# Performance work log

Measured on AMD Instinct MI355X. Metric: run time of the kernel, lower is better.

The kernel has to match this reference:

```python
import jax, jax.numpy as jnp
import numpy as np

B, N, NC = 16, 128, 32          # batch, num_vectors, num_condition_vectors
H, A, DEG = 256, 64, 3          # hidden_dim, attention_dim, degree
SCALE = float(np.sqrt(H) ** DEG)  # weights_scale = sqrt(hidden_dim)^degree = 4096
# S3 non-identity permutations lifted to batch tensor axes (batch axis 0 fixed)
PERMS = [(0, 1, 3, 2), (0, 2, 1, 3), (0, 2, 3, 1), (0, 3, 1, 2), (0, 3, 2, 1)]


def setup_inputs() -> dict:
    key = jax.random.key(0)
    ks = jax.random.split(key, 6)
    inv = 1.0 / np.sqrt(H)
    return {
        "x": jax.random.normal(ks[0], (B, N, H), jnp.float32),
        "x_mask": jnp.ones((B, N, 1), jnp.float32),
        "condition": jax.random.normal(ks[1], (B, NC, H), jnp.float32),
        "condition_mask": jnp.ones((B, NC, 1), jnp.float32),
        "W1": (jax.random.normal(ks[2], (DEG, H, H), jnp.float32) * inv),
        "b1": jnp.zeros((DEG, H), jnp.float32),
        "Wc": (jax.random.normal(ks[3], (DEG, H, H), jnp.float32) * inv),
        "Wlin": (jax.random.normal(ks[4], (DEG, H, A), jnp.float32) * inv),
        "blin": jnp.zeros((DEG, A), jnp.float32),
    }


def reference(x, x_mask, condition, condition_mask, W1, b1, Wc, Wlin, blin):
    # masked mean-pool of condition vectors: [B, H]
    pooled = (condition * condition_mask).sum(1) / jnp.maximum(condition_mask.sum(1), 1.0)
    ys, dvs = [], []
    for d in range(DEG):  # small fixed loop over structurally distinct branches
        dv = pooled @ Wc[d]                                   # daughter vector [B, H]
        h = jax.nn.gelu(x @ W1[d] + b1[d] + dv[:, None, :])   # branch encoder [B, N, H]
        y = (h @ Wlin[d] + blin[d]) * x_mask                  # linear + mask  [B, N, A]
        ys.append(y)
        dvs.append(dv)
    # degree-3 multilinear contraction: 'xbi,ybi,zbi->bxyz' == 'bxi,byi,bzi->bxyz'
    base = jnp.einsum('bxi,byi,bzi->bxyz', ys[0], ys[1], ys[2]) / SCALE
    # symmetrize: add all non-identity permuted views (S3 minus identity)
    out = base
    for p in PERMS:
        out = out + jnp.transpose(base, p)
    return out, jnp.stack(dvs)  # ([B,N,N,N], [DEG,B,H])
```

## Files before the change

### kernel.cpp

```cpp
#include <hip/hip_runtime.h>
#include <hip/hip_bf16.h>
#include <math.h>
#include <string.h>

#define BB   16
#define NN   128
#define NCC  32
#define HH   256
#define AA   64
#define DEGN 3
#define BNR  (BB*NN)

typedef __bf16 bf16x8 __attribute__((ext_vector_type(8)));
typedef float  f32x16 __attribute__((ext_vector_type(16)));

__device__ __forceinline__ unsigned int pk2(float lo, float hi) {
    __hip_bfloat162 h2 = __float22bfloat162_rn(make_float2(lo, hi));
    unsigned int u;
    memcpy(&u, &h2, 4);
    return u;
}
__device__ __forceinline__ unsigned short bfbits(float f) {
    __hip_bfloat16 h = __float2bfloat16(f);
    unsigned short u;
    memcpy(&u, &h, 2);
    return u;
}

__global__ __launch_bounds__(256) void k_head(const float* __restrict__ cond,
                                              const float* __restrict__ cmask,
                                              const float* __restrict__ Wc,
                                              const float* __restrict__ W1,
                                              const float* __restrict__ Wlin,
                                              float* __restrict__ dv,
                                              float* __restrict__ dv_out,
                                              unsigned short* __restrict__ W1t,
                                              unsigned short* __restrict__ Wlt) {
    __shared__ float shm[32 * 33];
    const int bid = blockIdx.x, t = threadIdx.x;

    if (bid < 48) {
        const int d = bid >> 4, b = bid & 15;
        float s = 0.f, ms = 0.f;
        for (int c = 0; c < NCC; ++c) {
            float mk = cmask[b * NCC + c];
            s  += cond[(b * NCC + c) * HH + t] * mk;
            ms += mk;
        }
        shm[t] = s / fmaxf(ms, 1.0f);
        __syncthreads();
        const float* Wd = Wc + (size_t)d * HH * HH;
        float acc = 0.f;
        for (int k = 0; k < HH; ++k) acc += shm[k] * Wd[k * HH + t];
        int idx = (d * BB + b) * HH + t;
        dv[idx]     = acc;
        dv_out[idx] = acc;
    } else if (bid < 240) {
        const int q = bid - 48;
        const int d = q >> 6, r2 = q & 63, tk = r2 >> 3, tn = r2 & 7;
        float (*tile)[33] = (float (*)[33])shm;
        #pragma unroll
        for (int p = 0; p < 4; ++p) {
            int kr = p * 8 + (t >> 5), nr = t & 31;
            tile[kr][nr] = W1[((size_t)d * HH + tk * 32 + kr) * HH + tn * 32 + nr];
        }
        __syncthreads();
        #pragma unroll
        for (int p = 0; p < 4; ++p) {
            int nr = p * 8 + (t >> 5), kr = t & 31;
            W1t[((size_t)d * HH + tn * 32 + nr) * HH + tk * 32 + kr] =
                bfbits(tile[kr][nr]);
        }
    } else {
        const int q = bid - 240;
        const int d = q >> 4, r3 = q & 15, tk = r3 >> 1, ta = r3 & 1;
        float (*tile)[33] = (float (*)[33])shm;
        #pragma unroll
        for (int p = 0; p < 4; ++p) {
            int kr = p * 8 + (t >> 5), ar = t & 31;
            tile[kr][ar] = Wlin[((size_t)d * HH + tk * 32 + kr) * AA + ta * 32 + ar];
        }
        __syncthreads();
        #pragma unroll
        for (int p = 0; p < 4; ++p) {
            int ar = p * 8 + (t >> 5), kr = t & 31;
            Wlt[((size_t)d * AA + ta * 32 + ar) * HH + tk * 32 + kr] =
                bfbits(tile[kr][ar]);
        }
    }
}

__global__ __launch_bounds__(256) void k_mlp(const float* __restrict__ x,
                                             const float* __restrict__ xmask,
                                             const float* __restrict__ b1,
                                             const float* __restrict__ blin,
                                             const float* __restrict__ dv,
                                             const unsigned short* __restrict__ W1t,
                                             const unsigned short* __restrict__ Wlt,
                                             float* __restrict__ yv) {
    __shared__ __align__(16) char ldsA[32 * 512];
    __shared__ float ps[2][32][68];

    const int t = threadIdx.x;
    const int d = blockIdx.x >> 6, rt = blockIdx.x & 63;
    const int row0 = rt * 32;
    const int b = row0 >> 7;
    const int lane = t & 63, wid = t >> 6;
    const int rl5 = lane & 31, h2v = lane >> 5;

    #pragma unroll
    for (int it = 0; it < 8; ++it) {
        const int r = wid * 8 + it;
        const float4 v = *(const float4*)&x[(size_t)(row0 + r) * HH + lane * 4];
        uint2 u = make_uint2(pk2(v.x, v.y), pk2(v.z, v.w));
        *(uint2*)(ldsA + r * 512 + ((lane * 8) ^ ((r & 7) << 4))) = u;
    }
    __syncthreads();

    f32x16 acc1[2];
    #pragma unroll
    for (int nt = 0; nt < 2; ++nt)
        #pragma unroll
        for (int e = 0; e < 16; ++e) acc1[nt][e] = 0.f;

    #pragma unroll
    for (int ks = 0; ks < 16; ++ks) {
        bf16x8 af = *(const bf16x8*)(ldsA + rl5 * 512 +
                      ((ks * 32 + h2v * 16) ^ ((rl5 & 7) << 4)));
        #pragma unroll
        for (int nt = 0; nt < 2; ++nt) {
            const int n = wid * 64 + nt * 32 + rl5;
            bf16x8 bf = *(const bf16x8*)(W1t +
                          ((size_t)d * HH + n) * HH + ks * 16 + h2v * 8);
            acc1[nt] = __builtin_amdgcn_mfma_f32_32x32x16_bf16(af, bf, acc1[nt], 0, 0, 0);
        }
    }
    __syncthreads();

    #pragma unroll
    for (int nt = 0; nt < 2; ++nt) {
        const int col = wid * 64 + nt * 32 + rl5;
        const float add = b1[d * HH + col] + dv[(d * BB + b) * HH + col];
        #pragma unroll
        for (int e = 0; e < 16; ++e) {
            const int row = (e & 3) + 8 * (e >> 2) + 4 * h2v;
            float v = acc1[nt][e] + add;
            float u = 0.7978845608028654f * (v + 0.044715f * v * v * v);
            float g = 0.5f * v * (1.0f + tanhf(u));
            *(unsigned short*)(ldsA + row * 512 + ((col * 2) ^ ((row & 7) << 4))) =
                bfbits(g);
        }
    }
    __syncthreads();

    const int qc = wid >> 1, kh = wid & 1;
    f32x16 acc2;
    #pragma unroll
    for (int e = 0; e < 16; ++e) acc2[e] = 0.f;
    #pragma unroll
    for (int ks = 0; ks < 8; ++ks) {
        const int kk = kh * 8 + ks;
        bf16x8 af = *(const bf16x8*)(ldsA + rl5 * 512 +
                      ((kk * 32 + h2v * 16) ^ ((rl5 & 7) << 4)));
        bf16x8 bf = *(const bf16x8*)(Wlt +
                      ((size_t)d * AA + qc * 32 + rl5) * HH + kk * 16 + h2v * 8);
        acc2 = __builtin_amdgcn_mfma_f32_32x32x16_bf16(af, bf, acc2, 0, 0, 0);
    }
    #pragma unroll
    for (int e = 0; e < 16; ++e) {
        const int row = (e & 3) + 8 * (e >> 2) + 4 * h2v;
        ps[kh][row][qc * 32 + rl5] = acc2[e];
    }
    __syncthreads();

    #pragma unroll
    for (int j = 0; j < 8; ++j) {
        const int idx = t * 8 + j;
        const int row = idx >> 6, a = idx & 63;
        float v = ps[0][row][a] + ps[1][row][a] + blin[d * AA + a];
        v *= xmask[row0 + row];
        yv[((size_t)d * BNR + row0 + row) * AA + a] = v;
    }
}

__device__ __forceinline__ void lds_fence_barrier() {
    asm volatile("s_waitcnt lgkmcnt(0)" ::: "memory");
    __builtin_amdgcn_s_barrier();
    __builtin_amdgcn_sched_barrier(0);
}
__device__ __forceinline__ void lds_wave_wait() {
    asm volatile("s_waitcnt lgkmcnt(0)" ::: "memory");
    __builtin_amdgcn_sched_barrier(0);
}

#define LROW 128

__global__ __launch_bounds__(256, 2) void k_contract(const float* __restrict__ yv,
                                                     float* __restrict__ outp) {
    __shared__ __align__(16) char lds[4 * 128 * LROW];
    char* A1b = lds;
    char* A2b = lds + 1 * 128 * LROW;
    char* B1b = lds + 2 * 128 * LROW;
    char* B2b = lds + 3 * 128 * LROW;

    const int t  = threadIdx.x;
    const int b  = blockIdx.x >> 5;
    const int xg = blockIdx.x & 31;

    const float* y0p = yv + (size_t)(0 * BNR + b * NN) * AA;
    const float* y1p = yv + (size_t)(1 * BNR + b * NN) * AA;
    const float* y2p = yv + (size_t)(2 * BNR + b * NN) * AA;

    const int lane = t & 63;
    const int wid  = t >> 6;
    const int li   = lane & 31;
    const int rh   = lane >> 5;

    #pragma unroll
    for (int it = 0; it < 16; ++it) {
        const int r   = wid * 32 + it * 2 + rh;
        const int swz = (r & 7) << 4;
        const float2 v1 = *(const float2*)&y1p[r * AA + 2 * li];
        const float2 v2 = *(const float2*)&y2p[r * AA + 2 * li];
        *(unsigned int*)(B1b + r * LROW + ((4 * li) ^ swz)) = pk2(v2.x, v2.y);
        *(unsigned int*)(B2b + r * LROW + ((4 * li) ^ swz)) = pk2(v1.x, v1.y);
    }

    const int rl5 = lane & 31, h2v = lane >> 5;
    const int wy  = wid * 32;
    const float inv = 1.0f / 4096.0f;

    char* s1 = A1b + wid * 4096;
    char* s2 = A2b + wid * 4096;

    for (int xi = 0; xi < 4; ++xi) {
        const int xr = xg * 4 + xi;
        const float s0 = y0p[xr * AA + lane];
        const float s1v = y1p[xr * AA + lane];
        const float s2v = y2p[xr * AA + lane];
        const float s0a = __shfl(s0, 2 * li),  s0b = __shfl(s0, 2 * li + 1);
        const float s1a = __shfl(s1v, 2 * li), s1b = __shfl(s1v, 2 * li + 1);
        const float s2a = __shfl(s2v, 2 * li), s2b = __shfl(s2v, 2 * li + 1);

        #pragma unroll
        for (int it = 0; it < 16; ++it) {
            const int r   = wid * 32 + it * 2 + rh;
            const int swz = (r & 7) << 4;
            const float2 v0 = *(const float2*)&y0p[r * AA + 2 * li];
            const float2 v1 = *(const float2*)&y1p[r * AA + 2 * li];
            unsigned int a1 = pk2(s0a * v1.x + s1a * v0.x, s0b * v1.y + s1b * v0.y);
            unsigned int a2 = pk2(s2a * v0.x, s2b * v0.y);
            *(unsigned int*)(A1b + r * LROW + ((4 * li) ^ swz)) = a1;
            *(unsigned int*)(A2b + r * LROW + ((4 * li) ^ swz)) = a2;
        }
        lds_fence_barrier();

        f32x16 acc[4];
        #pragma unroll
        for (int ni = 0; ni < 4; ++ni)
            #pragma unroll
            for (int e = 0; e < 16; ++e) acc[ni][e] = 0.f;

        #pragma unroll
        for (int p = 0; p < 4; ++p) {
            const char* Ua = (p == 0) ? A1b : (p == 1) ? B1b : (p == 2) ? A2b : B2b;
            const char* Va = (p == 0) ? B1b : (p == 1) ? A1b : (p == 2) ? B2b : A2b;
            #pragma unroll
            for (int ks = 0; ks < 4; ++ks) {
                const int arow = wy + rl5;
                bf16x8 af = *(const bf16x8*)(Ua + arow * LROW +
                              ((ks * 32 + h2v * 16) ^ ((arow & 7) << 4)));
                #pragma unroll
                for (int ni = 0; ni < 4; ++ni) {
                    const int brow = ni * 32 + rl5;
                    bf16x8 bf = *(const bf16x8*)(Va + brow * LROW +
                                  ((ks * 32 + h2v * 16) ^ ((brow & 7) << 4)));
                    acc[ni] = __builtin_amdgcn_mfma_f32_32x32x16_bf16(
                        af, bf, acc[ni], 0, 0, 0);
                }
            }
        }
        lds_fence_barrier();

        float* osl = outp + ((size_t)(b * NN + xr)) * (NN * NN);
        #pragma unroll
        for (int half = 0; half < 2; ++half) {
            #pragma unroll
            for (int ni = 0; ni < 4; ++ni) {
                const int colb = ni * 32 + rl5;
                #pragma unroll
                for (int e2 = 0; e2 < 8; ++e2) {
                    const int e    = half * 8 + e2;
                    const int rloc = (e2 & 3) + 8 * (e2 >> 2) + 4 * h2v;
                    char* reg = (e2 < 4) ? s1 : s2;
                    *(float*)(reg + ((rloc & 7) * 512) + colb * 4) =
                        acc[ni][e] * inv;
                }
            }
            lds_wave_wait();
            #pragma unroll
            for (int it2 = 0; it2 < 8; ++it2) {
                const int rloc = it2 * 2 + rh;
                const char* reg = (it2 < 4) ? s1 : s2;
                float4 v = *(const float4*)(reg + ((rloc & 7) * 512) + rl5 * 16);
                *(float4*)&osl[(size_t)(wy + half * 16 + rloc) * NN + rl5 * 4] = v;
            }
            lds_wave_wait();
        }
    }
}

extern "C" void kernel_launch(void* const* d_in, const int* in_sizes, int n_in,
                              void* d_out, int out_size, void* d_ws, size_t ws_size,
                              hipStream_t stream) {
    const float* x     = (const float*)d_in[0];
    const float* xmask = (const float*)d_in[1];
    const float* cond  = (const float*)d_in[2];
    const float* cmask = (const float*)d_in[3];
    const float* W1    = (const float*)d_in[4];
    const float* b1    = (const float*)d_in[5];
    const float* Wc    = (const float*)d_in[6];
    const float* Wlin  = (const float*)d_in[7];
    const float* blin  = (const float*)d_in[8];

    float* out = (float*)d_out;
    float* ws  = (float*)d_ws;

    float* dv  = ws;
    float* yv  = ws + 12288;
    unsigned short* W1t = (unsigned short*)((char*)d_ws + (size_t)(12288 + 393216) * 4);
    unsigned short* Wlt = W1t + (size_t)DEGN * HH * HH;
    float* dv_out = out + (size_t)BB * NN * NN * NN;

    k_head    <<<dim3(288), dim3(256), 0, stream>>>(cond, cmask, Wc, W1, Wlin,
                                                    dv, dv_out, W1t, Wlt);
    k_mlp     <<<dim3(DEGN * 64), dim3(256), 0, stream>>>(x, xmask, b1, blin, dv,
                                                          W1t, Wlt, yv);
    k_contract<<<dim3(BB * NN / 4), dim3(256), 0, stream>>>(yv, out);
}
```

Before: 57.35 us.

## Shrink contract LDS to three buffers and double grid for higher occupancy

The contraction kernel now reuses one A buffer for both symmetric operand terms, building the first one, running its MFMAs, then rebuilding the buffer for the second. This cuts LDS from four 16KB buffers to three. Launch bounds go from 2 to 4 blocks per CU, and each block handles 2 x-rows instead of 4, so there are twice as many blocks. The epilogue is restructured into four 8-row passes through a per-wave scratch area. In exchange, each x-row needs extra barriers and the B panels are loaded again per block, and the tighter register budget could cause spills of the 64 accumulator registers.

```diff
diff --git a/kernel.cpp b/kernel.cpp
--- a/kernel.cpp
+++ b/kernel.cpp
@@ -195,17 +195,16 @@
 
 #define LROW 128
 
-__global__ __launch_bounds__(256, 2) void k_contract(const float* __restrict__ yv,
+__global__ __launch_bounds__(256, 4) void k_contract(const float* __restrict__ yv,
                                                      float* __restrict__ outp) {
-    __shared__ __align__(16) char lds[4 * 128 * LROW];
-    char* A1b = lds;
-    char* A2b = lds + 1 * 128 * LROW;
-    char* B1b = lds + 2 * 128 * LROW;
-    char* B2b = lds + 3 * 128 * LROW;
+    __shared__ __align__(16) char lds[3 * 128 * LROW];
+    char* Ab  = lds;
+    char* B1b = lds + 1 * 128 * LROW;
+    char* B2b = lds + 2 * 128 * LROW;
 
     const int t  = threadIdx.x;
-    const int b  = blockIdx.x >> 5;
-    const int xg = blockIdx.x & 31;
+    const int b  = blockIdx.x >> 6;
+    const int xg = blockIdx.x & 63;
 
     const float* y0p = yv + (size_t)(0 * BNR + b * NN) * AA;
     const float* y1p = yv + (size_t)(1 * BNR + b * NN) * AA;
@@ -215,6 +214,8 @@
     const int wid  = t >> 6;
     const int li   = lane & 31;
     const int rh   = lane >> 5;
+    const int rl5  = lane & 31, h2v = lane >> 5;
+    const int wy   = wid * 32;
 
     #pragma unroll
     for (int it = 0; it < 16; ++it) {
@@ -226,15 +227,11 @@
         *(unsigned int*)(B2b + r * LROW + ((4 * li) ^ swz)) = pk2(v1.x, v1.y);
     }
 
-    const int rl5 = lane & 31, h2v = lane >> 5;
-    const int wy  = wid * 32;
     const float inv = 1.0f / 4096.0f;
-
-    char* s1 = A1b + wid * 4096;
-    char* s2 = A2b + wid * 4096;
-
-    for (int xi = 0; xi < 4; ++xi) {
-        const int xr = xg * 4 + xi;
+    char* scr = Ab + wid * 4096;
+
+    for (int xi = 0; xi < 2; ++xi) {
+        const int xr = xg * 2 + xi;
         const float s0 = y0p[xr * AA + lane];
         const float s1v = y1p[xr * AA + lane];
         const float s2v = y2p[xr * AA + lane];
@@ -242,68 +239,112 @@
         const float s1a = __shfl(s1v, 2 * li), s1b = __shfl(s1v, 2 * li + 1);
         const float s2a = __shfl(s2v, 2 * li), s2b = __shfl(s2v, 2 * li + 1);
 
+        f32x16 acc[4];
+        #pragma unroll
+        for (int ni = 0; ni < 4; ++ni)
+            #pragma unroll
+            for (int e = 0; e < 16; ++e) acc[ni][e] = 0.f;
+
         #pragma unroll
         for (int it = 0; it < 16; ++it) {
             const int r   = wid * 32 + it * 2 + rh;
             const int swz = (r & 7) << 4;
             const float2 v0 = *(const float2*)&y0p[r * AA + 2 * li];
             const float2 v1 = *(const float2*)&y1p[r * AA + 2 * li];
-            unsigned int a1 = pk2(s0a * v1.x + s1a * v0.x, s0b * v1.y + s1b * v0.y);
-            unsigned int a2 = pk2(s2a * v0.x, s2b * v0.y);
-            *(unsigned int*)(A1b + r * LROW + ((4 * li) ^ swz)) = a1;
-            *(unsigned int*)(A2b + r * LROW + ((4 * li) ^ swz)) = a2;
+            *(unsigned int*)(Ab + r * LROW + ((4 * li) ^ swz)) =
+                pk2(s0a * v1.x + s1a * v0.x, s0b * v1.y + s1b * v0.y);
         }
         lds_fence_barrier();
 
-        f32x16 acc[4];
-        #pragma unroll
-        for (int ni = 0; ni < 4; ++ni)
-            #pragma unroll
-            for (int e = 0; e < 16; ++e) acc[ni][e] = 0.f;
-
-        #pragma unroll
-        for (int p = 0; p < 4; ++p) {
-            const char* Ua = (p == 0) ? A1b : (p == 1) ? B1b : (p == 2) ? A2b : B2b;
-            const char* Va = (p == 0) ? B1b : (p == 1) ? A1b : (p == 2) ? B2b : A2b;
-            #pragma unroll
-            for (int ks = 0; ks < 4; ++ks) {
-                const int arow = wy + rl5;
-                bf16x8 af = *(const bf16x8*)(Ua + arow * LROW +
-                              ((ks * 32 + h2v * 16) ^ ((arow & 7) << 4)));
+        #pragma unroll
+        for (int ks = 0; ks < 4; ++ks) {
+            const int arow = wy + rl5;
+            bf16x8 af = *(const bf16x8*)(Ab + arow * LROW +
+                          ((ks * 32 + h2v * 16) ^ ((arow & 7) << 4)));
+            #pragma unroll
+            for (int ni = 0; ni < 4; ++ni) {
+                const int brow = ni * 32 + rl5;
+                bf16x8 bf = *(const bf16x8*)(B1b + brow * LROW +
+                              ((ks * 32 + h2v * 16) ^ ((brow & 7) << 4)));
+                acc[ni] = __builtin_amdgcn_mfma_f32_32x32x16_bf16(
+                    af, bf, acc[ni], 0, 0, 0);
+            }
+        }
+        #pragma unroll
+        for (int ks = 0; ks < 4; ++ks) {
+            const int arow = wy + rl5;
+            bf16x8 af = *(const bf16x8*)(B1b + arow * LROW +
+                          ((ks * 32 + h2v * 16) ^ ((arow & 7) << 4)));
+            #pragma unroll
+            for (int ni = 0; ni < 4; ++ni) {
+                const int brow = ni * 32 + rl5;
+                bf16x8 bf = *(const bf16x8*)(Ab + brow * LROW +
+                              ((ks * 32 + h2v * 16) ^ ((brow & 7) << 4)));
+                acc[ni] = __builtin_amdgcn_mfma_f32_32x32x16_bf16(
+                    af, bf, acc[ni], 0, 0, 0);
+            }
+        }
+        lds_fence_barrier();
+
+        #pragma unroll
+        for (int it = 0; it < 16; ++it) {
+            const int r   = wid * 32 + it * 2 + rh;
+            const int swz = (r & 7) << 4;
+            const float2 v0 = *(const float2*)&y0p[r * AA + 2 * li];
+            *(unsigned int*)(Ab + r * LROW + ((4 * li) ^ swz)) =
+                pk2(s2a * v0.x, s2b * v0.y);
+        }
+        lds_fence_barrier();
+
+        #pragma unroll
+        for (int ks = 0; ks < 4; ++ks) {
+            const int arow = wy + rl5;
+            bf16x8 af = *(const bf16x8*)(Ab + arow * LROW +
+                          ((ks * 32 + h2v * 16) ^ ((arow & 7) << 4)));
+            #pragma unroll
+            for (int ni = 0; ni < 4; ++ni) {
+                const int brow = ni * 32 + rl5;
+                bf16x8 bf = *(const bf16x8*)(B2b + brow * LROW +
+                              ((ks * 32 + h2v * 16) ^ ((brow & 7) << 4)));
+                acc[ni] = __builtin_amdgcn_mfma_f32_32x32x16_bf16(
+                    af, bf, acc[ni], 0, 0, 0);
+            }
+        }
+        #pragma unroll
+        for (int ks = 0; ks < 4; ++ks) {
+            const int arow = wy + rl5;
+            bf16x8 af = *(const bf16x8*)(B2b + arow * LROW +
+                          ((ks * 32 + h2v * 16) ^ ((arow & 7) << 4)));
+            #pragma unroll
+            for (int ni = 0; ni < 4; ++ni) {
+                const int brow = ni * 32 + rl5;
+                bf16x8 bf = *(const bf16x8*)(Ab + brow * LROW +
+                              ((ks * 32 + h2v * 16) ^ ((brow & 7) << 4)));
+                acc[ni] = __builtin_amdgcn_mfma_f32_32x32x16_bf16(
+                    af, bf, acc[ni], 0, 0, 0);
+            }
+        }
+        lds_fence_barrier();
+
+        float* osl = outp + ((size_t)(b * NN + xr)) * (NN * NN);
+        #pragma unroll
+        for (int q = 0; q < 4; ++q) {
+            #pragma unroll
+            for (int ni = 0; ni < 4; ++ni) {
                 #pragma unroll
-                for (int ni = 0; ni < 4; ++ni) {
-                    const int brow = ni * 32 + rl5;
-                    bf16x8 bf = *(const bf16x8*)(Va + brow * LROW +
-                                  ((ks * 32 + h2v * 16) ^ ((brow & 7) << 4)));
-                    acc[ni] = __builtin_amdgcn_mfma_f32_32x32x16_bf16(
-                        af, bf, acc[ni], 0, 0, 0);
-                }
-            }
-        }
-        lds_fence_barrier();
-
-        float* osl = outp + ((size_t)(b * NN + xr)) * (NN * NN);
-        #pragma unroll
-        for (int half = 0; half < 2; ++half) {
-            #pragma unroll
-            for (int ni = 0; ni < 4; ++ni) {
-                const int colb = ni * 32 + rl5;
-                #pragma unroll
-                for (int e2 = 0; e2 < 8; ++e2) {
-                    const int e    = half * 8 + e2;
-                    const int rloc = (e2 & 3) + 8 * (e2 >> 2) + 4 * h2v;
-                    char* reg = (e2 < 4) ? s1 : s2;
-                    *(float*)(reg + ((rloc & 7) * 512) + colb * 4) =
+                for (int j = 0; j < 4; ++j) {
+                    const int e    = q * 4 + j;
+                    const int srow = j + 4 * h2v;
+                    *(float*)(scr + srow * 512 + (ni * 32 + rl5) * 4) =
                         acc[ni][e] * inv;
                 }
             }
             lds_wave_wait();
             #pragma unroll
-            for (int it2 = 0; it2 < 8; ++it2) {
-                const int rloc = it2 * 2 + rh;
-                const char* reg = (it2 < 4) ? s1 : s2;
-                float4 v = *(const float4*)(reg + ((rloc & 7) * 512) + rl5 * 16);
-                *(float4*)&osl[(size_t)(wy + half * 16 + rloc) * NN + rl5 * 4] = v;
+            for (int it2 = 0; it2 < 4; ++it2) {
+                const int srow = it2 * 2 + rh;
+                float4 v = *(const float4*)(scr + srow * 512 + rl5 * 16);
+                *(float4*)&osl[(size_t)(wy + q * 8 + srow) * NN + rl5 * 4] = v;
             }
             lds_wave_wait();
         }
@@ -336,5 +377,5 @@
                                                     dv, dv_out, W1t, Wlt);
     k_mlp     <<<dim3(DEGN * 64), dim3(256), 0, stream>>>(x, xmask, b1, blin, dv,
                                                           W1t, Wlt, yv);
-    k_contract<<<dim3(BB * NN / 4), dim3(256), 0, stream>>>(yv, out);
-}
+    k_contract<<<dim3(BB * NN / 2), dim3(256), 0, stream>>>(yv, out);
+}
```

After: 71.10 us. +24.0%, slower.
